# Performance work log

Measured on AMD Instinct MI355X. Metric: run time of the kernel, lower is better.

Reference implementation:

```python
import jax, jax.numpy as jnp
import numpy as np

B, N_CH, NUM_CLASSES, H, W, MAX_BOXES = 4, 3, 20, 512, 512, 50


def setup_inputs() -> dict:
    key = jax.random.key(0)
    k1, k2, k3, k4, k5, k6, k7, k8 = jax.random.split(key, 8)
    y_fcn = jax.random.normal(k1, (B, N_CH * NUM_CLASSES, H, W), dtype=jnp.float32)
    im_data = jax.random.normal(k2, (B, N_CH, H, W), dtype=jnp.float32)
    im_info = jnp.ones((B, 3), dtype=jnp.float32)
    # valid boxes: x1 < x2 <= W, y1 < y2 <= H, class in [0, NUM_CLASSES)
    x1 = jax.random.randint(k3, (B, MAX_BOXES), 0, W // 2)
    y1 = jax.random.randint(k4, (B, MAX_BOXES), 0, H // 2)
    bw = jax.random.randint(k5, (B, MAX_BOXES), 1, W // 2)
    bh = jax.random.randint(k6, (B, MAX_BOXES), 1, H // 2)
    cls = jax.random.randint(k7, (B, MAX_BOXES), 0, NUM_CLASSES)
    gt_boxes = jnp.stack([x1, y1, x1 + bw, y1 + bh, cls], axis=-1).astype(jnp.int32)
    num_boxes = jax.random.randint(k8, (B,), 1, MAX_BOXES + 1).astype(jnp.int32)
    return {"y_fcn": y_fcn, "im_data": im_data, "im_info": im_info,
            "gt_boxes": gt_boxes, "num_boxes": num_boxes}


def reference(y_fcn, im_data, im_info, gt_boxes, num_boxes):
    b, n, h, w = im_data.shape
    num_classes = y_fcn.shape[1] // n
    # per-pixel squared error between im_data and each class's n-channel slice
    yf = y_fcn.reshape(b, num_classes, n, h, w)            # class c occupies channels [c*n, (c+1)*n)
    D = jnp.sum((im_data[:, None] - yf) ** 2, axis=2)       # [B, C, H, W]
    # 2D integral image (padded) so every box sum is 4 gathers instead of a crop
    P = jnp.cumsum(jnp.cumsum(D, axis=-2), axis=-1)
    P = jnp.pad(P, ((0, 0), (0, 0), (1, 0), (1, 0)))        # [B, C, H+1, W+1]
    x1, y1, x2, y2, cls = (gt_boxes[..., i] for i in range(5))
    bidx = jnp.arange(b)[:, None]
    corner = lambda yy, xx: P[bidx, cls, yy, xx]
    box_sum = corner(y2, x2) - corner(y1, x2) - corner(y2, x1) + corner(y1, x1)
    area = (y2 - y1) * (x2 - x1)                             # [B, MAX_BOXES]
    valid = jnp.arange(gt_boxes.shape[1])[None, :] < num_boxes[:, None]
    denom = (n * jnp.maximum(area, 1)).astype(box_sum.dtype)
    err = jnp.where(valid, box_sum / denom, 0.0)
    return jnp.sum(err) / num_boxes.sum().astype(err.dtype)
```

## Files before the change

kernel.cpp:

```cpp
#include <hip/hip_runtime.h>

#define BATCH 4
#define N_CH 3
#define NUM_CLASSES 20
#define IMG_H 512
#define IMG_W 512
#define MAX_BOXES 50
#define NSLOTS (BATCH * MAX_BOXES)
#define PARTS 16
#define BLOCK 256
#define TOTAL_BLOCKS (NSLOTS * PARTS)

__global__ __launch_bounds__(BLOCK)
void box_err_kernel(const float* __restrict__ y_fcn,
                    const float* __restrict__ im_data,
                    const int*   __restrict__ gt_boxes,
                    const int*   __restrict__ num_boxes,
                    float*       __restrict__ ws_part) {
    const int slot = blockIdx.x / PARTS;
    const int part = blockIdx.x % PARTS;
    const int b    = slot / MAX_BOXES;
    const int box  = slot % MAX_BOXES;
    const int tid  = (int)threadIdx.x;

    const int* g  = gt_boxes + slot * 5;
    const int x1 = g[0], y1 = g[1], x2 = g[2], y2 = g[3], cls = g[4];
    const int bh = y2 - y1;
    const int c0 = x1 & ~3;
    const int n4 = (x2 - c0 + 3) >> 2;

    const int nrows = (part < bh) ? ((bh - part + PARTS - 1) / PARTS) : 0;
    const int vmax  = (box < num_boxes[b]) ? nrows * n4 : 0;

    const int plane = IMG_H * IMG_W;
    const float* im = im_data + (size_t)b * N_CH * plane;
    const float* yf = y_fcn + ((size_t)b * NUM_CLASSES + cls) * (size_t)(N_CH * plane);

    float s = 0.0f;
    for (int v = tid; v < vmax; v += BLOCK) {
        const int rl  = v / n4;
        const int ic  = v - rl * n4;
        const int row = y1 + part + rl * PARTS;
        const int cc  = c0 + (ic << 2);
        const int base = row * IMG_W + cc;
        const float m0 = (cc + 0 >= x1 && cc + 0 < x2) ? 1.0f : 0.0f;
        const float m1 = (cc + 1 >= x1 && cc + 1 < x2) ? 1.0f : 0.0f;
        const float m2 = (cc + 2 >= x1 && cc + 2 < x2) ? 1.0f : 0.0f;
        const float m3 = (cc + 3 >= x1 && cc + 3 < x2) ? 1.0f : 0.0f;
        #pragma unroll
        for (int nn = 0; nn < N_CH; ++nn) {
            const float4 a = *(const float4*)(im + nn * plane + base);
            const float4 q = *(const float4*)(yf + nn * plane + base);
            float d;
            d = (a.x - q.x) * m0; s = fmaf(d, d, s);
            d = (a.y - q.y) * m1; s = fmaf(d, d, s);
            d = (a.z - q.z) * m2; s = fmaf(d, d, s);
            d = (a.w - q.w) * m3; s = fmaf(d, d, s);
        }
    }

    #pragma unroll
    for (int off = 32; off > 0; off >>= 1)
        s += __shfl_down(s, off, 64);

    __shared__ float red[BLOCK / 64];
    if ((tid & 63) == 0) red[tid >> 6] = s;
    __syncthreads();
    if (tid == 0)
        ws_part[blockIdx.x] = red[0] + red[1] + red[2] + red[3];
}

__global__ __launch_bounds__(BLOCK)
void finalize_kernel(const float* __restrict__ ws_part,
                     const int*   __restrict__ gt_boxes,
                     const int*   __restrict__ num_boxes,
                     float*       __restrict__ out) {
    const int t = (int)threadIdx.x;
    float e = 0.0f;
    if (t < NSLOTS) {
        const int b   = t / MAX_BOXES;
        const int box = t % MAX_BOXES;
        if (box < num_boxes[b]) {
            const float4* p = (const float4*)(ws_part + t * PARTS);
            float4 s0 = p[0], s1 = p[1], s2 = p[2], s3 = p[3];
            const float sum = (s0.x + s0.y + s0.z + s0.w)
                            + (s1.x + s1.y + s1.z + s1.w)
                            + (s2.x + s2.y + s2.z + s2.w)
                            + (s3.x + s3.y + s3.z + s3.w);
            const int* g = gt_boxes + t * 5;
            const int area = (g[2] - g[0]) * (g[3] - g[1]);
            e = sum / (float)(N_CH * max(area, 1));
        }
    }
    #pragma unroll
    for (int off = 32; off > 0; off >>= 1)
        e += __shfl_down(e, off, 64);

    __shared__ float red[BLOCK / 64];
    if ((t & 63) == 0) red[t >> 6] = e;
    __syncthreads();
    if (t == 0) {
        int nb = 0;
        #pragma unroll
        for (int bb = 0; bb < BATCH; ++bb) nb += num_boxes[bb];
        out[0] = (red[0] + red[1] + red[2] + red[3]) / (float)nb;
    }
}

extern "C" void kernel_launch(void* const* d_in, const int* in_sizes, int n_in,
                              void* d_out, int out_size, void* d_ws, size_t ws_size,
                              hipStream_t stream) {
    const float* y_fcn     = (const float*)d_in[0];
    const float* im_data   = (const float*)d_in[1];
    const int*   gt_boxes  = (const int*)d_in[3];
    const int*   num_boxes = (const int*)d_in[4];
    float* out     = (float*)d_out;
    float* ws_part = (float*)d_ws;

    box_err_kernel<<<TOTAL_BLOCKS, BLOCK, 0, stream>>>(
        y_fcn, im_data, gt_boxes, num_boxes, ws_part);

    finalize_kernel<<<1, BLOCK, 0, stream>>>(ws_part, gt_boxes, num_boxes, out);
}
```

Measured before the change: 12.62 us.

## Double row partitions per box and remap blocks so each XCD owns contiguous slots

Splits each box's rows across 32 blocks instead of 16, doubling the grid so more work is in flight per box. Block indices are also remapped so that the round-robin block-to-XCD dispatch gives each XCD a contiguous range of box slots, keeping the same box's data within one XCD's L2. The finalize kernel now sums 32 partials per slot. This adds more blocks (many with little or no work for small boxes) and relies on the dispatch order being round-robin across 8 XCDs.

```diff
diff --git a/kernel.cpp b/kernel.cpp
--- a/kernel.cpp
+++ b/kernel.cpp
@@ -7,7 +7,9 @@
 #define IMG_W 512
 #define MAX_BOXES 50
 #define NSLOTS (BATCH * MAX_BOXES)
-#define PARTS 16
+#define PARTS 32
+#define NXCD 8
+#define SLOTS_PER_XCD (NSLOTS / NXCD)
 #define BLOCK 256
 #define TOTAL_BLOCKS (NSLOTS * PARTS)
 
@@ -17,8 +19,11 @@
                     const int*   __restrict__ gt_boxes,
                     const int*   __restrict__ num_boxes,
                     float*       __restrict__ ws_part) {
-    const int slot = blockIdx.x / PARTS;
-    const int part = blockIdx.x % PARTS;
+    const int d    = (int)blockIdx.x;
+    const int r    = d & (NXCD - 1);
+    const int q    = d >> 3;
+    const int slot = r * SLOTS_PER_XCD + (q >> 5);
+    const int part = q & (PARTS - 1);
     const int b    = slot / MAX_BOXES;
     const int box  = slot % MAX_BOXES;
     const int tid  = (int)threadIdx.x;
@@ -50,12 +55,12 @@
         #pragma unroll
         for (int nn = 0; nn < N_CH; ++nn) {
             const float4 a = *(const float4*)(im + nn * plane + base);
-            const float4 q = *(const float4*)(yf + nn * plane + base);
-            float d;
-            d = (a.x - q.x) * m0; s = fmaf(d, d, s);
-            d = (a.y - q.y) * m1; s = fmaf(d, d, s);
-            d = (a.z - q.z) * m2; s = fmaf(d, d, s);
-            d = (a.w - q.w) * m3; s = fmaf(d, d, s);
+            const float4 q4 = *(const float4*)(yf + nn * plane + base);
+            float dd;
+            dd = (a.x - q4.x) * m0; s = fmaf(dd, dd, s);
+            dd = (a.y - q4.y) * m1; s = fmaf(dd, dd, s);
+            dd = (a.z - q4.z) * m2; s = fmaf(dd, dd, s);
+            dd = (a.w - q4.w) * m3; s = fmaf(dd, dd, s);
         }
     }
 
@@ -67,7 +72,7 @@
     if ((tid & 63) == 0) red[tid >> 6] = s;
     __syncthreads();
     if (tid == 0)
-        ws_part[blockIdx.x] = red[0] + red[1] + red[2] + red[3];
+        ws_part[slot * PARTS + part] = red[0] + red[1] + red[2] + red[3];
 }
 
 __global__ __launch_bounds__(BLOCK)
@@ -82,11 +87,12 @@
         const int box = t % MAX_BOXES;
         if (box < num_boxes[b]) {
             const float4* p = (const float4*)(ws_part + t * PARTS);
-            float4 s0 = p[0], s1 = p[1], s2 = p[2], s3 = p[3];
-            const float sum = (s0.x + s0.y + s0.z + s0.w)
-                            + (s1.x + s1.y + s1.z + s1.w)
-                            + (s2.x + s2.y + s2.z + s2.w)
-                            + (s3.x + s3.y + s3.z + s3.w);
+            float sum = 0.0f;
+            #pragma unroll
+            for (int k = 0; k < PARTS / 4; ++k) {
+                const float4 s4 = p[k];
+                sum += (s4.x + s4.y) + (s4.z + s4.w);
+            }
             const int* g = gt_boxes + t * 5;
             const int area = (g[2] - g[0]) * (g[3] - g[1]);
             e = sum / (float)(N_CH * max(area, 1));
```

Result: slower. 15.43 us (+22.3%).
